# Kernel tuning notes

Measured on AMD Instinct MI355X. Metric: run time of the kernel, lower is better.

The kernel has to match this reference:

```python
import jax, jax.numpy as jnp
import numpy as np

N, E, D_IN, HID, OUT, H = 20000, 320000, 128, 128, 128, 4

def _lin(key, fan_in, fan_out):
    kw, kb = jax.random.split(key)
    W = jax.random.normal(kw, (fan_in, fan_out), jnp.float32) * 0.05
    b = jax.random.normal(kb, (fan_out,), jnp.float32) * 0.05
    return W, b

def setup_inputs() -> dict:
    key = jax.random.key(0)
    ks = jax.random.split(key, 10)
    x = jax.random.normal(ks[0], (N, D_IN), jnp.float32)
    edge_index = jax.random.randint(ks[1], (2, E), 0, N, jnp.int32)
    # Layer 0: TransformerConv(D_IN -> HID, heads=H, concat=True)
    Wq0, bq0 = _lin(ks[2], D_IN, H * HID)
    Wk0, bk0 = _lin(ks[3], D_IN, H * HID)
    Wv0, bv0 = _lin(ks[4], D_IN, H * HID)
    Ws0, bs0 = _lin(ks[5], D_IN, H * HID)   # root/skip projection
    # Layer 1: TransformerConv(H*HID -> OUT, heads=H, concat=False)
    Wq1, bq1 = _lin(ks[6], H * HID, H * OUT)
    Wk1, bk1 = _lin(ks[7], H * HID, H * OUT)
    Wv1, bv1 = _lin(ks[8], H * HID, H * OUT)
    Ws1, bs1 = _lin(ks[9], H * HID, OUT)    # skip maps to OUT when concat=False
    return dict(x=x, edge_index=edge_index,
                Wq0=Wq0, bq0=bq0, Wk0=Wk0, bk0=bk0, Wv0=Wv0, bv0=bv0, Ws0=Ws0, bs0=bs0,
                Wq1=Wq1, bq1=bq1, Wk1=Wk1, bk1=bk1, Wv1=Wv1, bv1=bv1, Ws1=Ws1, bs1=bs1)

def _transformer_conv(x, src, dst, Wq, bq, Wk, bk, Wv, bv, Ws, bs, heads, out_ch, concat):
    n = x.shape[0]
    q = (x @ Wq + bq).reshape(n, heads, out_ch)
    k = (x @ Wk + bk).reshape(n, heads, out_ch)
    v = (x @ Wv + bv).reshape(n, heads, out_ch)
    # per-edge attention logits: [E, H]
    alpha = jnp.einsum('ehc,ehc->eh', q[dst], k[src]) / jnp.sqrt(jnp.float32(out_ch))
    # softmax grouped by destination node (numerically stable)
    m = jax.ops.segment_max(alpha, dst, num_segments=n)        # [N, H]
    alpha = jnp.exp(alpha - m[dst])
    s = jax.ops.segment_sum(alpha, dst, num_segments=n)       # [N, H]
    alpha = alpha / (s[dst] + 1e-16)
    # weighted scatter-add of messages: [N, H, C]
    out = jax.ops.segment_sum(alpha[..., None] * v[src], dst, num_segments=n)
    if concat:
        out = out.reshape(n, heads * out_ch)
    else:
        out = out.mean(axis=1)
    return out + x @ Ws + bs  # root weight (skip connection)

def reference(x, edge_index,
              Wq0, bq0, Wk0, bk0, Wv0, bv0, Ws0, bs0,
              Wq1, bq1, Wk1, bk1, Wv1, bv1, Ws1, bs1):
    src, dst = edge_index[0], edge_index[1]
    h = _transformer_conv(x, src, dst, Wq0, bq0, Wk0, bk0, Wv0, bv0, Ws0, bs0, H, HID, True)
    h = jax.nn.relu(h)  # dropout is identity in eval mode
    out = _transformer_conv(h, src, dst, Wq1, bq1, Wk1, bk1, Wv1, bv1, Ws1, bs1, H, OUT, False)
    return out
```

## Files before the change

### kernel.cpp

```cpp
#include <hip/hip_runtime.h>
#include <hip/hip_bf16.h>
#include <math.h>

#define HCH    512
#define OUTD   128
#define N0CAT  2048
#define N1CAT  1664
#define P0STR  1024
#define P1STR  640
#define KVW    1024
#define DCAP   64

typedef __attribute__((ext_vector_type(8))) short short8v;
typedef __attribute__((ext_vector_type(8))) unsigned short ushort8v;
typedef __attribute__((ext_vector_type(4))) unsigned short ushort4v;
typedef __attribute__((ext_vector_type(4))) float floatx4;
typedef __attribute__((ext_vector_type(2))) float floatx2;
typedef __attribute__((ext_vector_type(4))) unsigned int uintx4;

__device__ inline float bf2f(unsigned short u) {
    return __uint_as_float(((unsigned)u) << 16);
}

__device__ inline unsigned short f2bf(float f) {
    return (unsigned short)__bfloat16_as_ushort(__float2bfloat16(f));
}

template <bool HI>
__device__ inline floatx2 fp8x2_to_f32(unsigned int w) {
    return __builtin_amdgcn_cvt_pk_f32_fp8(w, HI);
}

__device__ inline unsigned int f32x4_to_fp8(float a, float b, float c, float d) {
    int w = __builtin_amdgcn_cvt_pk_fp8_f32(a, b, 0, false);
    w = __builtin_amdgcn_cvt_pk_fp8_f32(c, d, w, true);
    return (unsigned int)w;
}

__device__ inline void gload_lds16(const void* g, void* l) {
    __builtin_amdgcn_global_load_lds(
        (const __attribute__((address_space(1))) unsigned int*)g,
        (__attribute__((address_space(3))) unsigned int*)l, 16, 0, 0);
}


__device__ void tpose_tile(const float* __restrict__ W, __hip_bfloat16* __restrict__ o,
                           int K, int C, int bx, int by, int t, float (*tile)[33]) {
    int c0 = bx * 32, k0 = by * 32;
    int tx = t & 31, ty = t >> 5;
    #pragma unroll
    for (int r = ty; r < 32; r += 8)
        tile[r][tx] = W[(size_t)(k0 + r) * C + c0 + tx];
    __syncthreads();
    #pragma unroll
    for (int r = ty; r < 32; r += 8)
        o[(size_t)(c0 + r) * K + k0 + tx] = __float2bfloat16(tile[tx][r]);
}

__global__ __launch_bounds__(256) void prep_all(
        const float* __restrict__ x, __hip_bfloat16* __restrict__ Xb,
        const float* __restrict__ Wq0, const float* __restrict__ Wk0,
        const float* __restrict__ Wv0, const float* __restrict__ Ws0,
        const float* __restrict__ Wq1, const float* __restrict__ Wk1,
        const float* __restrict__ Wv1, const float* __restrict__ Ws1,
        const float* __restrict__ bq0, const float* __restrict__ bk0,
        const float* __restrict__ bv0, const float* __restrict__ bs0,
        const float* __restrict__ bq1, const float* __restrict__ bk1,
        const float* __restrict__ bv1, const float* __restrict__ bs1,
        __hip_bfloat16* __restrict__ Wc0, __hip_bfloat16* __restrict__ Wc1,
        float* __restrict__ bc0, float* __restrict__ bc1,
        int* __restrict__ deg, int* __restrict__ srcs,
        const int* __restrict__ srce, const int* __restrict__ dste,
        int N, int E) {
    __shared__ float tile[32][33];
    int t = threadIdx.x;
    int b = blockIdx.x;
    int nb_cast = (N * 128 + 255) >> 8;
    if (b < nb_cast) {
        int i = b * 256 + t;
        if (i < N * 128) Xb[i] = __float2bfloat16(x[i]);
        return;
    }
    b -= nb_cast;
    if (b < 256) {
        int z = b >> 6, rem = b & 63;
        const float* W = (z == 0) ? Wq0 : (z == 1) ? Wk0 : (z == 2) ? Wv0 : Ws0;
        tpose_tile(W, Wc0 + (size_t)z * 512 * 128, 128, 512, rem & 15, rem >> 4, t, tile);
        return;
    }
    b -= 256;
    if (b < 768) {
        int z = b >> 8, rem = b & 255;
        const float* W = (z == 0) ? Wq1 : (z == 1) ? Wk1 : Wv1;
        tpose_tile(W, Wc1 + (size_t)z * 512 * 512, 512, 512, rem & 15, rem >> 4, t, tile);
        return;
    }
    b -= 768;
    if (b < 64) {
        tpose_tile(Ws1, Wc1 + (size_t)1536 * 512, 512, 128, b & 3, b >> 2, t, tile);
        return;
    }
    b -= 64;
    if (b < 8) {
        int i = b * 256 + t;
        if (i < N0CAT) {
            int sel = i >> 9, col = i & 511;
            const float* bb = (sel == 0) ? bq0 : (sel == 1) ? bk0 : (sel == 2) ? bv0 : bs0;
            bc0[i] = bb[col];
        }
        if (i < N1CAT) {
            if (i < 1536) {
                int sel = i >> 9, col = i & 511;
                const float* bb = (sel == 0) ? bq1 : (sel == 1) ? bk1 : bv1;
                bc1[i] = bb[col];
            } else {
                bc1[i] = bs1[i - 1536];
            }
        }
        return;
    }
    b -= 8;
    {
        int e = b * 256 + t;
        if (e < E) {
            int d = dste[e];
            int pos = atomicAdd(&deg[d], 1);
            if (pos < DCAP) srcs[d * DCAP + pos] = srce[e];
        }
    }
}


#define BM 128
#define BN 128
#define BK 64
#define TILEB (BM * BK * 2)

__global__ __launch_bounds__(256) void gemm_mfma(const __hip_bfloat16* __restrict__ A,
                                                 const __hip_bfloat16* __restrict__ Bt,
                                                 const float* __restrict__ bias,
                                                 __hip_bfloat16* __restrict__ P,
                                                 int pstride,
                                                 unsigned char* __restrict__ KV8,
                                                 int M, int K, int Nd, int mt_pad) {
    __shared__ __hip_bfloat16 As[2][BM][BK];
    __shared__ __hip_bfloat16 Bs[2][BN][BK];
    int f = blockIdx.x;
    int mt = f % mt_pad, nt = f / mt_pad;
    int bm = mt * BM, bn = nt * BN;
    if (bm >= M) return;
    int t = threadIdx.x;
    int lane = t & 63, w = t >> 6;
    int quad = lane >> 4, l16 = lane & 15;
    int wm = (w >> 1) * 64, wn = (w & 1) * 64;

    int srow = w * 8 + (lane >> 3);
    int c8g = (lane & 7) ^ ((lane >> 3) & 7);
    const char* Ab = (const char*)(A + (size_t)(bm + srow) * K + c8g * 8);
    const char* Bb = (const char*)(Bt + (size_t)(bn + srow) * K + c8g * 8);
    char* Al = (char*)&As[0][0][0] + w * 1024;
    char* Bl = (char*)&Bs[0][0][0] + w * 1024;

    int sw = l16 & 7;

    floatx4 acc[4][4];
    #pragma unroll
    for (int i = 0; i < 4; i++)
        #pragma unroll
        for (int j = 0; j < 4; j++)
            acc[i][j] = (floatx4)0.0f;

    auto issue_tile = [&](int k0, int bsel) {
        #pragma unroll
        for (int i = 0; i < 4; i++) {
            size_t go = ((size_t)i * 32 * K + k0) * 2;
            gload_lds16(Ab + go, Al + bsel * TILEB + i * 4096);
            gload_lds16(Bb + go, Bl + bsel * TILEB + i * 4096);
        }
    };

    issue_tile(0, 0);
    int nk = K / BK;
    for (int tt = 0; tt < nk; tt++) {
        int cur = tt & 1;
        if (tt + 1 < nk) {
            issue_tile((tt + 1) * BK, cur ^ 1);
            asm volatile("s_waitcnt vmcnt(8)" ::: "memory");
        } else {
            asm volatile("s_waitcnt vmcnt(0)" ::: "memory");
        }
        __builtin_amdgcn_s_barrier();
        __builtin_amdgcn_sched_barrier(0);
        __builtin_amdgcn_s_setprio(1);
        #pragma unroll
        for (int ks = 0; ks < BK; ks += 32) {
            int c8a = (quad + (ks >> 3)) ^ sw;
            short8v af[4], bfr[4];
            #pragma unroll
            for (int i = 0; i < 4; i++)
                af[i] = *(const short8v*)&As[cur][wm + i * 16 + l16][c8a * 8];
            #pragma unroll
            for (int j = 0; j < 4; j++)
                bfr[j] = *(const short8v*)&Bs[cur][wn + j * 16 + l16][c8a * 8];
            #pragma unroll
            for (int i = 0; i < 4; i++)
                #pragma unroll
                for (int j = 0; j < 4; j++)
                    acc[i][j] = __builtin_amdgcn_mfma_f32_16x16x32_bf16(bfr[j], af[i], acc[i][j], 0, 0, 0);
        }
        __builtin_amdgcn_s_setprio(0);
        __builtin_amdgcn_sched_barrier(0);
        __builtin_amdgcn_s_barrier();
        __builtin_amdgcn_sched_barrier(0);
    }

    #pragma unroll
    for (int i = 0; i < 4; i++) {
        int row = bm + wm + i * 16 + l16;
        if (row >= M) continue;
        #pragma unroll
        for (int j = 0; j < 4; j++) {
            int col = bn + wn + j * 16 + quad * 4;
            floatx4 bv = *(const floatx4*)(bias + col);
            float v0 = acc[i][j][0] + bv[0];
            float v1 = acc[i][j][1] + bv[1];
            float v2 = acc[i][j][2] + bv[2];
            float v3 = acc[i][j][3] + bv[3];
            if (col < 512) {
                ushort4v o = { f2bf(v0), f2bf(v1), f2bf(v2), f2bf(v3) };
                *(ushort4v*)(P + (size_t)row * pstride + col) = o;
            } else if (col < 1024) {
                int b = col - 512;
                int nb = ((b >> 3) << 4) + (b & 7);
                *(unsigned int*)(KV8 + (size_t)row * KVW + nb) = f32x4_to_fp8(v0, v1, v2, v3);
            } else if (col < 1536) {
                int b = col - 1024;
                int nb = ((b >> 3) << 4) + 8 + (b & 7);
                *(unsigned int*)(KV8 + (size_t)row * KVW + nb) = f32x4_to_fp8(v0, v1, v2, v3);
            } else {
                ushort4v o = { f2bf(v0), f2bf(v1), f2bf(v2), f2bf(v3) };
                *(ushort4v*)(P + (size_t)row * pstride + 512 + (col - 1536)) = o;
            }
        }
    }
}


#define PF 4

__global__ __launch_bounds__(256) void attn_kernel(const __hip_bfloat16* __restrict__ P,
                                                   int pstride,
                                                   const unsigned char* __restrict__ KV8,
                                                   const int* __restrict__ deg,
                                                   const int* __restrict__ srcs,
                                                   __hip_bfloat16* __restrict__ out_b,
                                                   float* __restrict__ out_f,
                                                   int n_nodes, int mode) {
    int wave = threadIdx.x >> 6;
    int lane = threadIdx.x & 63;
    int node = blockIdx.x * 4 + wave;
    if (node >= n_nodes) return;
    const float qsc = 0.08838834764831845f * 1.4426950408889634f;

    const __hip_bfloat16* Prow = P + (size_t)node * pstride;
    floatx2 q2[4];
    {
        ushort8v qu = *(const ushort8v*)(Prow + lane * 8);
        #pragma unroll
        for (int j = 0; j < 4; j++) {
            q2[j][0] = bf2f(qu[2 * j])     * qsc;
            q2[j][1] = bf2f(qu[2 * j + 1]) * qsc;
        }
    }

    float l = 0.f;
    floatx2 acc2[4];
    #pragma unroll
    for (int j = 0; j < 4; j++) acc2[j] = (floatx2)0.0f;

    int cnt = deg[node];
    if (cnt > DCAP) cnt = DCAP;
    const int* ep = srcs + (size_t)node * DCAP;
    const unsigned char* Kb = KV8 + lane * 16;

    uintx4 kv[PF];
    #pragma unroll
    for (int i = 0; i < PF; i++) {
        if (i < cnt) {
            int s = ep[i];
            kv[i] = *(const uintx4*)(Kb + (size_t)s * KVW);
        }
    }

    int e = 0;
    for (; e + PF <= cnt; e += PF) {
        #pragma unroll
        for (int i = 0; i < PF; i++) {
            uintx4 u = kv[i];
            int pe = e + i + PF;
            if (pe < cnt) {
                int s = ep[pe];
                kv[i] = *(const uintx4*)(Kb + (size_t)s * KVW);
            }
            floatx2 k01 = fp8x2_to_f32<false>(u[0]);
            floatx2 k23 = fp8x2_to_f32<true >(u[0]);
            floatx2 k45 = fp8x2_to_f32<false>(u[1]);
            floatx2 k67 = fp8x2_to_f32<true >(u[1]);
            floatx2 d2 = q2[0] * k01;
            d2 += q2[1] * k23;
            d2 += q2[2] * k45;
            d2 += q2[3] * k67;
            float part = d2[0] + d2[1];
            part += __shfl_xor(part, 1);
            part += __shfl_xor(part, 2);
            part += __shfl_xor(part, 4);
            part += __shfl_xor(part, 8);
            float p = exp2f(part);
            l += p;
            floatx2 pv = { p, p };
            floatx2 v01 = fp8x2_to_f32<false>(u[2]);
            floatx2 v23 = fp8x2_to_f32<true >(u[2]);
            floatx2 v45 = fp8x2_to_f32<false>(u[3]);
            floatx2 v67 = fp8x2_to_f32<true >(u[3]);
            acc2[0] += pv * v01;
            acc2[1] += pv * v23;
            acc2[2] += pv * v45;
            acc2[3] += pv * v67;
        }
    }
    #pragma unroll
    for (int i = 0; i < PF; i++) {
        if (e + i < cnt) {
            uintx4 u = kv[i];
            floatx2 k01 = fp8x2_to_f32<false>(u[0]);
            floatx2 k23 = fp8x2_to_f32<true >(u[0]);
            floatx2 k45 = fp8x2_to_f32<false>(u[1]);
            floatx2 k67 = fp8x2_to_f32<true >(u[1]);
            floatx2 d2 = q2[0] * k01;
            d2 += q2[1] * k23;
            d2 += q2[2] * k45;
            d2 += q2[3] * k67;
            float part = d2[0] + d2[1];
            part += __shfl_xor(part, 1);
            part += __shfl_xor(part, 2);
            part += __shfl_xor(part, 4);
            part += __shfl_xor(part, 8);
            float p = exp2f(part);
            l += p;
            floatx2 pv = { p, p };
            floatx2 v01 = fp8x2_to_f32<false>(u[2]);
            floatx2 v23 = fp8x2_to_f32<true >(u[2]);
            floatx2 v45 = fp8x2_to_f32<false>(u[3]);
            floatx2 v67 = fp8x2_to_f32<true >(u[3]);
            acc2[0] += pv * v01;
            acc2[1] += pv * v23;
            acc2[2] += pv * v45;
            acc2[3] += pv * v67;
        }
    }
    float inv = (l > 0.f) ? 1.f / l : 0.f;

    if (mode == 0) {
        ushort8v su = *(const ushort8v*)(Prow + 512 + lane * 8);
        ushort8v o;
        #pragma unroll
        for (int j = 0; j < 8; j++) {
            float r = fmaxf(acc2[j >> 1][j & 1] * inv + bf2f(su[j]), 0.f);
            o[j] = f2bf(r);
        }
        *(ushort8v*)(out_b + (size_t)node * HCH + lane * 8) = o;
    } else {
        float r[8];
        #pragma unroll
        for (int j = 0; j < 8; j++) {
            r[j] = acc2[j >> 1][j & 1] * inv;
            r[j] += __shfl_xor(r[j], 16);
            r[j] += __shfl_xor(r[j], 32);
            r[j] *= 0.25f;
        }
        if (lane < 16) {
            const __hip_bfloat16* sp = Prow + 512 + lane * 8;
            float* op = out_f + (size_t)node * OUTD + lane * 8;
            #pragma unroll
            for (int j = 0; j < 8; j++) op[j] = r[j] + bf2f(__bfloat16_as_ushort(sp[j]));
        }
    }
}


static inline size_t align256(size_t x) { return (x + 255) & ~(size_t)255; }

extern "C" void kernel_launch(void* const* d_in, const int* in_sizes, int n_in,
                              void* d_out, int out_size, void* d_ws, size_t ws_size,
                              hipStream_t stream) {
    const float* x   = (const float*)d_in[0];
    const int*   ei  = (const int*)d_in[1];
    const float* Wq0 = (const float*)d_in[2];  const float* bq0 = (const float*)d_in[3];
    const float* Wk0 = (const float*)d_in[4];  const float* bk0 = (const float*)d_in[5];
    const float* Wv0 = (const float*)d_in[6];  const float* bv0 = (const float*)d_in[7];
    const float* Ws0 = (const float*)d_in[8];  const float* bs0 = (const float*)d_in[9];
    const float* Wq1 = (const float*)d_in[10]; const float* bq1 = (const float*)d_in[11];
    const float* Wk1 = (const float*)d_in[12]; const float* bk1 = (const float*)d_in[13];
    const float* Wv1 = (const float*)d_in[14]; const float* bv1 = (const float*)d_in[15];
    const float* Ws1 = (const float*)d_in[16]; const float* bs1 = (const float*)d_in[17];
    float* out = (float*)d_out;

    const int N = in_sizes[0] / 128;
    const int E = in_sizes[1] / 2;
    const int* src = ei;
    const int* dst = ei + E;

    int mtiles = (N + BM - 1) / BM;
    int mt_pad = (mtiles + 7) & ~7;
    const int Mpad = mt_pad * BM;

    char* ws = (char*)d_ws;
    __hip_bfloat16* P0  = (__hip_bfloat16*)ws; ws += align256((size_t)N * P0STR * 2);
    __hip_bfloat16* P1  = P0;
    __hip_bfloat16* Hbb = (__hip_bfloat16*)ws; ws += align256((size_t)Mpad * HCH * 2);
    __hip_bfloat16* Xb  = (__hip_bfloat16*)ws; ws += align256((size_t)Mpad * 128 * 2);
    unsigned char* KV8  = (unsigned char*)ws;  ws += align256((size_t)N * KVW);
    __hip_bfloat16* Wc0 = (__hip_bfloat16*)ws; ws += align256((size_t)N0CAT * 128 * 2);
    __hip_bfloat16* Wc1 = (__hip_bfloat16*)ws; ws += align256((size_t)N1CAT * 512 * 2);
    float* bc0 = (float*)ws; ws += align256((size_t)N0CAT * 4);
    float* bc1 = (float*)ws; ws += align256((size_t)N1CAT * 4);
    int* deg    = (int*)ws; ws += align256((size_t)N * 4);
    int* srcs   = (int*)ws; ws += align256((size_t)N * DCAP * 4);

    dim3 blk(256);

    hipMemsetAsync(deg, 0, (size_t)N * 4, stream);

    int nb_cast = (N * 128 + 255) / 256;
    int nb_bucket = (E + 255) / 256;
    int nb_prep = nb_cast + 256 + 768 + 64 + 8 + nb_bucket;
    prep_all<<<nb_prep, blk, 0, stream>>>(
        x, Xb, Wq0, Wk0, Wv0, Ws0, Wq1, Wk1, Wv1, Ws1,
        bq0, bk0, bv0, bs0, bq1, bk1, bv1, bs1,
        Wc0, Wc1, bc0, bc1, deg, srcs, src, dst, N, E);

    gemm_mfma<<<dim3(mt_pad * (N0CAT / BN)), blk, 0, stream>>>(
        Xb, Wc0, bc0, P0, P0STR, KV8, N, 128, N0CAT, mt_pad);
    attn_kernel<<<(N + 3) / 4, blk, 0, stream>>>(P0, P0STR, KV8, deg, srcs, Hbb, nullptr, N, 0);

    gemm_mfma<<<dim3(mt_pad * (N1CAT / BN)), blk, 0, stream>>>(
        Hbb, Wc1, bc1, P1, P1STR, KV8, N, 512, N1CAT, mt_pad);
    attn_kernel<<<(N + 3) / 4, blk, 0, stream>>>(P1, P1STR, KV8, deg, srcs, nullptr, out, N, 1);
}
```

Before: 332.1 us.

## Pre-permute K/V weight columns and single-buffer GEMM LDS tiles

```diff
diff --git a/kernel.cpp b/kernel.cpp
--- a/kernel.cpp
+++ b/kernel.cpp
@@ -45,7 +45,8 @@
 
 
 __device__ void tpose_tile(const float* __restrict__ W, __hip_bfloat16* __restrict__ o,
-                           int K, int C, int bx, int by, int t, float (*tile)[33]) {
+                           int K, int C, int bx, int by, int t, float (*tile)[33],
+                           int pmode) {
     int c0 = bx * 32, k0 = by * 32;
     int tx = t & 31, ty = t >> 5;
     #pragma unroll
@@ -53,8 +54,11 @@
         tile[r][tx] = W[(size_t)(k0 + r) * C + c0 + tx];
     __syncthreads();
     #pragma unroll
-    for (int r = ty; r < 32; r += 8)
-        o[(size_t)(c0 + r) * K + k0 + tx] = __float2bfloat16(tile[tx][r]);
+    for (int r = ty; r < 32; r += 8) {
+        int col = c0 + r;
+        if (pmode) col = ((col >> 3) << 4) + (col & 7) + ((pmode == 2) ? 8 : 0);
+        o[(size_t)col * K + k0 + tx] = __float2bfloat16(tile[tx][r]);
+    }
 }
 
 __global__ __launch_bounds__(256) void prep_all(
@@ -85,19 +89,23 @@
     if (b < 256) {
         int z = b >> 6, rem = b & 63;
         const float* W = (z == 0) ? Wq0 : (z == 1) ? Wk0 : (z == 2) ? Wv0 : Ws0;
-        tpose_tile(W, Wc0 + (size_t)z * 512 * 128, 128, 512, rem & 15, rem >> 4, t, tile);
+        int base = (z == 0) ? 0 : (z == 3) ? 1536 : 512;
+        int pmode = (z == 1) ? 1 : (z == 2) ? 2 : 0;
+        tpose_tile(W, Wc0 + (size_t)base * 128, 128, 512, rem & 15, rem >> 4, t, tile, pmode);
         return;
     }
     b -= 256;
     if (b < 768) {
         int z = b >> 8, rem = b & 255;
         const float* W = (z == 0) ? Wq1 : (z == 1) ? Wk1 : Wv1;
-        tpose_tile(W, Wc1 + (size_t)z * 512 * 512, 512, 512, rem & 15, rem >> 4, t, tile);
+        int base = (z == 0) ? 0 : 512;
+        int pmode = (z == 1) ? 1 : (z == 2) ? 2 : 0;
+        tpose_tile(W, Wc1 + (size_t)base * 512, 512, 512, rem & 15, rem >> 4, t, tile, pmode);
         return;
     }
     b -= 768;
     if (b < 64) {
-        tpose_tile(Ws1, Wc1 + (size_t)1536 * 512, 512, 128, b & 3, b >> 2, t, tile);
+        tpose_tile(Ws1, Wc1 + (size_t)1536 * 512, 512, 128, b & 3, b >> 2, t, tile, 0);
         return;
     }
     b -= 64;
@@ -106,13 +114,18 @@
         if (i < N0CAT) {
             int sel = i >> 9, col = i & 511;
             const float* bb = (sel == 0) ? bq0 : (sel == 1) ? bk0 : (sel == 2) ? bv0 : bs0;
-            bc0[i] = bb[col];
+            int d = (sel == 0) ? i
+                  : (sel == 3) ? i
+                  : 512 + ((col >> 3) << 4) + (col & 7) + ((sel == 2) ? 8 : 0);
+            bc0[d] = bb[col];
         }
         if (i < N1CAT) {
             if (i < 1536) {
                 int sel = i >> 9, col = i & 511;
                 const float* bb = (sel == 0) ? bq1 : (sel == 1) ? bk1 : bv1;
-                bc1[i] = bb[col];
+                int d = (sel == 0) ? i
+                      : 512 + ((col >> 3) << 4) + (col & 7) + ((sel == 2) ? 8 : 0);
+                bc1[d] = bb[col];
             } else {
                 bc1[i] = bs1[i - 1536];
             }
@@ -134,7 +147,6 @@
 #define BM 128
 #define BN 128
 #define BK 64
-#define TILEB (BM * BK * 2)
 
 __global__ __launch_bounds__(256) void gemm_mfma(const __hip_bfloat16* __restrict__ A,
                                                  const __hip_bfloat16* __restrict__ Bt,
@@ -143,8 +155,8 @@
                                                  int pstride,
                                                  unsigned char* __restrict__ KV8,
                                                  int M, int K, int Nd, int mt_pad) {
-    __shared__ __hip_bfloat16 As[2][BM][BK];
-    __shared__ __hip_bfloat16 Bs[2][BN][BK];
+    __shared__ __hip_bfloat16 As[BM][BK];
+    __shared__ __hip_bfloat16 Bs[BN][BK];
     int f = blockIdx.x;
     int mt = f % mt_pad, nt = f / mt_pad;
     int bm = mt * BM, bn = nt * BN;
@@ -158,8 +170,8 @@
     int c8g = (lane & 7) ^ ((lane >> 3) & 7);
     const char* Ab = (const char*)(A + (size_t)(bm + srow) * K + c8g * 8);
     const char* Bb = (const char*)(Bt + (size_t)(bn + srow) * K + c8g * 8);
-    char* Al = (char*)&As[0][0][0] + w * 1024;
-    char* Bl = (char*)&Bs[0][0][0] + w * 1024;
+    char* Al = (char*)&As[0][0] + w * 1024;
+    char* Bl = (char*)&Bs[0][0] + w * 1024;
 
     int sw = l16 & 7;
 
@@ -170,48 +182,31 @@
         for (int j = 0; j < 4; j++)
             acc[i][j] = (floatx4)0.0f;
 
-    auto issue_tile = [&](int k0, int bsel) {
+    for (int k0 = 0; k0 < K; k0 += BK) {
+        __syncthreads();
         #pragma unroll
         for (int i = 0; i < 4; i++) {
             size_t go = ((size_t)i * 32 * K + k0) * 2;
-            gload_lds16(Ab + go, Al + bsel * TILEB + i * 4096);
-            gload_lds16(Bb + go, Bl + bsel * TILEB + i * 4096);
-        }
-    };
-
-    issue_tile(0, 0);
-    int nk = K / BK;
-    for (int tt = 0; tt < nk; tt++) {
-        int cur = tt & 1;
-        if (tt + 1 < nk) {
-            issue_tile((tt + 1) * BK, cur ^ 1);
-            asm volatile("s_waitcnt vmcnt(8)" ::: "memory");
-        } else {
-            asm volatile("s_waitcnt vmcnt(0)" ::: "memory");
-        }
-        __builtin_amdgcn_s_barrier();
-        __builtin_amdgcn_sched_barrier(0);
-        __builtin_amdgcn_s_setprio(1);
+            gload_lds16(Ab + go, Al + i * 4096);
+            gload_lds16(Bb + go, Bl + i * 4096);
+        }
+        __syncthreads();
         #pragma unroll
         for (int ks = 0; ks < BK; ks += 32) {
             int c8a = (quad + (ks >> 3)) ^ sw;
             short8v af[4], bfr[4];
             #pragma unroll
             for (int i = 0; i < 4; i++)
-                af[i] = *(const short8v*)&As[cur][wm + i * 16 + l16][c8a * 8];
+                af[i] = *(const short8v*)&As[wm + i * 16 + l16][c8a * 8];
             #pragma unroll
             for (int j = 0; j < 4; j++)
-                bfr[j] = *(const short8v*)&Bs[cur][wn + j * 16 + l16][c8a * 8];
+                bfr[j] = *(const short8v*)&Bs[wn + j * 16 + l16][c8a * 8];
             #pragma unroll
             for (int i = 0; i < 4; i++)
                 #pragma unroll
                 for (int j = 0; j < 4; j++)
                     acc[i][j] = __builtin_amdgcn_mfma_f32_16x16x32_bf16(bfr[j], af[i], acc[i][j], 0, 0, 0);
         }
-        __builtin_amdgcn_s_setprio(0);
-        __builtin_amdgcn_sched_barrier(0);
-        __builtin_amdgcn_s_barrier();
-        __builtin_amdgcn_sched_barrier(0);
     }
 
     #pragma unroll
@@ -229,14 +224,8 @@
             if (col < 512) {
                 ushort4v o = { f2bf(v0), f2bf(v1), f2bf(v2), f2bf(v3) };
                 *(ushort4v*)(P + (size_t)row * pstride + col) = o;
-            } else if (col < 1024) {
-                int b = col - 512;
-                int nb = ((b >> 3) << 4) + (b & 7);
-                *(unsigned int*)(KV8 + (size_t)row * KVW + nb) = f32x4_to_fp8(v0, v1, v2, v3);
             } else if (col < 1536) {
-                int b = col - 1024;
-                int nb = ((b >> 3) << 4) + 8 + (b & 7);
-                *(unsigned int*)(KV8 + (size_t)row * KVW + nb) = f32x4_to_fp8(v0, v1, v2, v3);
+                *(unsigned int*)(KV8 + (size_t)row * KVW + (col - 512)) = f32x4_to_fp8(v0, v1, v2, v3);
             } else {
                 ushort4v o = { f2bf(v0), f2bf(v1), f2bf(v2), f2bf(v3) };
                 *(ushort4v*)(P + (size_t)row * pstride + 512 + (col - 1536)) = o;
```

Result: faster. 317.0 us (-4.6%).
